# Optimization experiments

Measured on AMD Instinct MI355X. Metric: run time of the kernel, lower is better.

Reference implementation:

```python
import jax, jax.numpy as jnp
import numpy as np

V = 6890   # SMPL vertices
K = 24     # joints
NB = 10    # shape betas
NP = 207   # pose blendshape basis = 23*9
PARENTS = np.array([-1, 0, 0, 0, 1, 2, 3, 4, 5, 6, 7, 8, 9, 9, 9, 12, 13, 14, 16, 17, 18, 19, 20, 21])


def setup_inputs() -> dict:
    key = jax.random.key(0)
    ks = jax.random.split(key, 8)
    B = 1024
    body_pose = jax.random.normal(ks[0], (B, 69), dtype=jnp.float32) * 0.2
    betas = jax.random.normal(ks[1], (B, NB), dtype=jnp.float32)
    global_orient = jax.random.normal(ks[2], (B, 3), dtype=jnp.float32) * 0.2
    v_template = jax.random.normal(ks[3], (V, 3), dtype=jnp.float32) * 0.1
    shapedirs = jax.random.normal(ks[4], (V, 3, NB), dtype=jnp.float32) * 0.01
    posedirs = jax.random.normal(ks[5], (NP, V * 3), dtype=jnp.float32) * 0.01
    J_regressor = jax.nn.softmax(jax.random.normal(ks[6], (K, V), dtype=jnp.float32), axis=-1)
    lbs_weights = jax.nn.softmax(jax.random.normal(ks[7], (V, K), dtype=jnp.float32) * 4.0, axis=-1)
    parents = jnp.asarray(PARENTS, dtype=jnp.int32)
    return dict(body_pose=body_pose, betas=betas, global_orient=global_orient,
                v_template=v_template, shapedirs=shapedirs, posedirs=posedirs,
                J_regressor=J_regressor, lbs_weights=lbs_weights, parents=parents)


def _rodrigues(aa):
    # aa: [..., 3] axis-angle -> [..., 3, 3] rotation matrices
    angle = jnp.linalg.norm(aa + 1e-8, axis=-1, keepdims=True)  # [...,1]
    axis = aa / angle
    sin = jnp.sin(angle)[..., None]
    cos = jnp.cos(angle)[..., None]
    rx, ry, rz = axis[..., 0], axis[..., 1], axis[..., 2]
    z = jnp.zeros_like(rx)
    Km = jnp.stack([z, -rz, ry, rz, z, -rx, -ry, rx, z], axis=-1).reshape(aa.shape[:-1] + (3, 3))
    ident = jnp.eye(3, dtype=aa.dtype)
    return ident + sin * Km + (1.0 - cos) * (Km @ Km)


def reference(body_pose, betas, global_orient, v_template, shapedirs, posedirs,
              J_regressor, lbs_weights, parents):
    full_pose = jnp.concatenate([global_orient, body_pose], axis=1)  # [B,72]
    B = betas.shape[0]
    dtype = betas.dtype

    # shape blend shapes
    v_shaped = v_template + jnp.einsum('bl,vkl->bvk', betas, shapedirs)  # [B,V,3]
    # rest joints
    joints_t = jnp.einsum('jv,bvk->bjk', J_regressor, v_shaped)          # [B,K,3]

    # pose -> rotation matrices (pose2rot=True path)
    rot_mats = _rodrigues(full_pose.reshape(B, K, 3))                    # [B,K,3,3]

    # pose blend shapes
    ident = jnp.eye(3, dtype=dtype)
    pose_feature = (rot_mats[:, 1:] - ident).reshape(B, NP)              # [B,207]
    v_posed = v_shaped + (pose_feature @ posedirs).reshape(B, V, 3)

    # kinematic chain (batch_rigid_transform)
    rel_joints = joints_t.at[:, 1:].add(-joints_t[:, PARENTS[1:]])       # [B,K,3]
    tm = jnp.concatenate([rot_mats, rel_joints[..., None]], axis=-1)     # [B,K,3,4]
    bottom = jnp.broadcast_to(jnp.array([0., 0., 0., 1.], dtype=dtype), (B, K, 1, 4))
    tm = jnp.concatenate([tm, bottom], axis=-2)                          # [B,K,4,4]
    chain = [tm[:, 0]]
    for i in range(1, K):  # fixed small kinematic tree
        chain.append(chain[PARENTS[i]] @ tm[:, i])
    transforms = jnp.stack(chain, axis=1)                                # [B,K,4,4]
    joints = transforms[..., :3, 3]                                      # posed joints

    # relative transforms: subtract rotated rest-joint position
    A = transforms.at[..., :3, 3].add(
        -jnp.einsum('bkij,bkj->bki', transforms[..., :3, :3], joints_t))  # [B,K,4,4]

    # linear blend skinning
    T = jnp.einsum('vk,bkij->bvij', lbs_weights, A)                      # [B,V,4,4]
    vertices = jnp.einsum('bvij,bvj->bvi', T[..., :3, :3], v_posed) + T[..., :3, 3]
    return vertices, joints_t, joints, rot_mats
```

## Files before the change

### kernel.cpp

```cpp
#include <hip/hip_runtime.h>
#include <hip/hip_bf16.h>

#define VNUM 6890
#define KJ 24
#define NBETA 10
#define NPOSE 207
#define KPAD 224
#define BATCH 1024
#define N3 20670
#define NVG 431
#define NROWF 20688

#define OUT_V  0
#define OUT_JT 21166080
#define OUT_J  21239808
#define OUT_RM 21313536

#define WS_JVJS 0
#define WS_ABFF 792
#define WS_WBFF 262936
#define WS_PFBF 373528
#define WS_PDTF 488216

typedef unsigned short ushort;
typedef __attribute__((ext_vector_type(8))) short short8v;
typedef __attribute__((ext_vector_type(4))) float floatx4;

__device__ __forceinline__ ushort f2bfu(float x) {
  __hip_bfloat16 h = __float2bfloat16(x);
  union { __hip_bfloat16 h; ushort u; } cv; cv.h = h; return cv.u;
}

__global__ __launch_bounds__(256) void jreg_kernel(
    const float* __restrict__ Jr, const float* __restrict__ vt,
    const float* __restrict__ sd, float* __restrict__ JvJs) {
  const int j = blockIdx.x;
  const int chunk = blockIdx.y;
  const int t = threadIdx.x;
  const int lane = t & 63, wid = t >> 6;
  const int vbeg = chunk * 1723;
  const int vend = (vbeg + 1723 < VNUM) ? vbeg + 1723 : VNUM;
  __shared__ float red[4][33];
  float acc[33];
#pragma unroll
  for (int q = 0; q < 33; q++) acc[q] = 0.0f;
  for (int v = vbeg + t; v < vend; v += 256) {
    float r = Jr[j * VNUM + v];
    const float* vtp = vt + v * 3;
    const float* sdp = sd + v * 30;
    acc[0] += r * vtp[0];
    acc[1] += r * vtp[1];
    acc[2] += r * vtp[2];
#pragma unroll
    for (int q = 0; q < 30; q++) acc[3 + q] += r * sdp[q];
  }
#pragma unroll
  for (int q = 0; q < 33; q++) {
    float x = acc[q];
    for (int off = 32; off > 0; off >>= 1) x += __shfl_down(x, off, 64);
    if (lane == 0) red[wid][q] = x;
  }
  __syncthreads();
  if (t < 33)
    atomicAdd(&JvJs[j * 33 + t], red[0][t] + red[1][t] + red[2][t] + red[3][t]);
}

__global__ __launch_bounds__(64) void batch_prep(
    const float* __restrict__ body_pose, const float* __restrict__ betas,
    const float* __restrict__ global_orient, const float* __restrict__ JvJs,
    float* __restrict__ out_jt, float* __restrict__ out_j, float* __restrict__ out_rm,
    ushort* __restrict__ pfbf, ushort* __restrict__ Abff) {
  const int b = blockIdx.x;
  const int t = threadIdx.x;
  __shared__ float R[24][9];
  __shared__ float jt[24][3];
  __shared__ float chR[24][9];
  __shared__ float cht[24][3];

  if (t < 24) {
    float ax, ay, az;
    if (t == 0) {
      ax = global_orient[b * 3 + 0];
      ay = global_orient[b * 3 + 1];
      az = global_orient[b * 3 + 2];
    } else {
      const float* p = body_pose + (size_t)b * 69 + (t - 1) * 3;
      ax = p[0]; ay = p[1]; az = p[2];
    }
    float px = ax + 1e-8f, py = ay + 1e-8f, pz = az + 1e-8f;
    float angle = sqrtf(px * px + py * py + pz * pz);
    float inv = 1.0f / angle;
    float rx = ax * inv, ry = ay * inv, rz = az * inv;
    float s = sinf(angle), c = cosf(angle);
    float cc = 1.0f - c;
    float m[9];
    m[0] = 1.0f - cc * (ry * ry + rz * rz);
    m[1] = -s * rz + cc * rx * ry;
    m[2] =  s * ry + cc * rx * rz;
    m[3] =  s * rz + cc * rx * ry;
    m[4] = 1.0f - cc * (rx * rx + rz * rz);
    m[5] = -s * rx + cc * ry * rz;
    m[6] = -s * ry + cc * rx * rz;
    m[7] =  s * rx + cc * ry * rz;
    m[8] = 1.0f - cc * (rx * rx + ry * ry);
#pragma unroll
    for (int e = 0; e < 9; e++) {
      R[t][e] = m[e];
      out_rm[(size_t)b * 216 + t * 9 + e] = m[e];
    }
  }
  for (int idx = t; idx < 72; idx += 64) {
    int j = idx / 3, c = idx % 3;
    const float* JJ = JvJs + j * 33;
    float s = JJ[c];
    const float* be = betas + (size_t)b * NBETA;
#pragma unroll
    for (int l = 0; l < NBETA; l++) s += be[l] * JJ[3 + c * 10 + l];
    jt[j][c] = s;
    out_jt[(size_t)b * 72 + idx] = s;
  }
  __syncthreads();
  for (int mI = t; mI < KPAD; mI += 64) {
    float val = 0.0f;
    if (mI < NPOSE) {
      int k = 1 + mI / 9, e = mI % 9;
      val = R[k][e] - ((e == 0 || e == 4 || e == 8) ? 1.0f : 0.0f);
    } else if (mI < NPOSE + NBETA) {
      val = betas[(size_t)b * NBETA + (mI - NPOSE)];
    }
    int kb = mI >> 5, quad = (mI >> 3) & 3, j = mI & 7;
    pfbf[(size_t)(((b >> 4) * 7 + kb) * 512) + (quad * 16 + (b & 15)) * 8 + j] =
        f2bfu(val);
  }
  if (t == 0) {
    const int par[24] = {-1, 0, 0, 0, 1, 2, 3, 4, 5, 6, 7, 8, 9, 9, 9, 12, 13, 14, 16, 17, 18, 19, 20, 21};
#pragma unroll
    for (int e = 0; e < 9; e++) chR[0][e] = R[0][e];
    cht[0][0] = jt[0][0]; cht[0][1] = jt[0][1]; cht[0][2] = jt[0][2];
    for (int k = 1; k < 24; k++) {
      int p = par[k];
      float rel0 = jt[k][0] - jt[p][0];
      float rel1 = jt[k][1] - jt[p][1];
      float rel2 = jt[k][2] - jt[p][2];
#pragma unroll
      for (int i = 0; i < 3; i++) {
        float a0 = chR[p][i * 3 + 0], a1 = chR[p][i * 3 + 1], a2 = chR[p][i * 3 + 2];
        chR[k][i * 3 + 0] = a0 * R[k][0] + a1 * R[k][3] + a2 * R[k][6];
        chR[k][i * 3 + 1] = a0 * R[k][1] + a1 * R[k][4] + a2 * R[k][7];
        chR[k][i * 3 + 2] = a0 * R[k][2] + a1 * R[k][5] + a2 * R[k][8];
        cht[k][i] = a0 * rel0 + a1 * rel1 + a2 * rel2 + cht[p][i];
      }
    }
  }
  __syncthreads();
  if (t < 24) {
    int k = t;
#pragma unroll
    for (int i = 0; i < 3; i++) out_j[(size_t)b * 72 + k * 3 + i] = cht[k][i];
  }
  for (int e = t; e < 512; e += 64) {
    int quad = e >> 7, n = (e >> 3) & 15, j = e & 7;
    int k = quad * 8 + j;
    float val = 0.0f;
    if (n < 12 && k < 24) {
      int i = n >> 2, jj = n & 3;
      if (jj < 3) {
        val = chR[k][i * 3 + jj];
      } else {
        val = cht[k][i] - (chR[k][i * 3 + 0] * jt[k][0] +
                           chR[k][i * 3 + 1] * jt[k][1] +
                           chR[k][i * 3 + 2] * jt[k][2]);
      }
    }
    Abff[(size_t)b * 512 + e] = f2bfu(val);
  }
}

__global__ __launch_bounds__(256) void transpose_pd(
    const float* __restrict__ pd, ushort* __restrict__ pdTf,
    const float* __restrict__ sd,
    const float* __restrict__ w, ushort* __restrict__ wbff) {
  {
    int lb = blockIdx.y * 324 + blockIdx.x;
    if (lb < 864) {
      int i = lb * 256 + threadIdx.x;
      int vg = i >> 9, e = i & 511;
      int quad = e >> 7, l15 = (e >> 3) & 15, j = e & 7;
      int v = vg * 16 + l15, k = quad * 8 + j;
      float x = (v < VNUM && k < 24) ? w[v * 24 + k] : 0.0f;
      wbff[i] = f2bfu(x);
    }
  }
  __shared__ float tile[32][65];
  const int t = threadIdx.x;
  const int n0 = blockIdx.x * 64;
  const int k0 = blockIdx.y * 32;
  const int c = t & 63;
  for (int r = t >> 6; r < 32; r += 4) {
    int k = k0 + r, n = n0 + c;
    float x = 0.0f;
    if (n < N3) {
      if (k < NPOSE) x = pd[(size_t)k * N3 + n];
      else if (k < NPOSE + NBETA) x = sd[(size_t)n * 10 + (k - NPOSE)];
    }
    tile[r][c] = x;
  }
  __syncthreads();
  const int n = t >> 2;
  const int j0 = (t & 3) * 8;
  const int rg = n0 + n;
  if (rg >= NROWF) return;
  unsigned int outw[4];
#pragma unroll
  for (int jj = 0; jj < 4; jj++) {
    unsigned int lo = f2bfu(tile[j0 + jj * 2][n]);
    unsigned int hi = f2bfu(tile[j0 + jj * 2 + 1][n]);
    outw[jj] = lo | (hi << 16);
  }
  const int vg = rg / 48;
  const int rl = rg - vg * 48;
  const int ns = rl >> 4, l15 = rl & 15;
  const int kb = k0 >> 5, quad = j0 >> 3;
  *(uint4*)&pdTf[(size_t)(((vg * 3 + ns) * 7 + kb) * 512) + (quad * 16 + l15) * 8] =
      make_uint4(outw[0], outw[1], outw[2], outw[3]);
}

__global__ __launch_bounds__(256, 2) void fused_mfma(
    const ushort* __restrict__ pfbf, const ushort* __restrict__ pdTf,
    const float* __restrict__ vt, const ushort* __restrict__ wbff,
    const ushort* __restrict__ Abff, float* __restrict__ out_v) {
  __shared__ __align__(16) ushort AbS[32 * 512];
  __shared__ float vpS[4][32 * 50];
  const int tid = threadIdx.x;
  const int lane = tid & 63, wv = tid >> 6;
  const int l15 = lane & 15, quad = lane >> 4;

  const int bid = blockIdx.x;
  const int L = (bid & 7) * 432 + (bid >> 3);
  const int bt = L & 31;
  const int q  = L >> 5;
  const int bm = bt * 32;
  const int vg = q * 4 + wv;
  const int vgc = (vg < NVG) ? vg : (NVG - 1);

  short8v ab[8];
  {
    const ushort* asrc = Abff + (size_t)(bm + wv * 8) * 512 + lane * 8;
#pragma unroll
    for (int j = 0; j < 8; j++) ab[j] = *(const short8v*)(asrc + j * 512);
  }

  const short8v wf = *(const short8v*)(wbff + (size_t)vgc * 512 + lane * 8);
  const int gn0 = vgc * 48 + l15;
  float vt0 = (gn0      < N3) ? vt[gn0]      : 0.0f;
  float vt1 = (gn0 + 16 < N3) ? vt[gn0 + 16] : 0.0f;
  float vt2 = (gn0 + 32 < N3) ? vt[gn0 + 32] : 0.0f;

  const ushort* apf0 = pfbf + (size_t)((bm >> 4) * 7) * 512 + lane * 8;
  const ushort* apf1 = apf0 + 7 * 512;
  const ushort* bpf  = pdTf + (size_t)(vgc * 21) * 512 + lane * 8;

  const floatx4 zero = {0.0f, 0.0f, 0.0f, 0.0f};
  floatx4 acc[2][3];
#pragma unroll
  for (int bg = 0; bg < 2; bg++)
#pragma unroll
    for (int ns = 0; ns < 3; ns++) acc[bg][ns] = zero;

#pragma unroll
  for (int kb = 0; kb < 7; kb++) {
    short8v a0 = *(const short8v*)(apf0 + kb * 512);
    short8v a1 = *(const short8v*)(apf1 + kb * 512);
    short8v b0 = *(const short8v*)(bpf + (0 * 7 + kb) * 512);
    short8v b1 = *(const short8v*)(bpf + (1 * 7 + kb) * 512);
    short8v b2 = *(const short8v*)(bpf + (2 * 7 + kb) * 512);
    acc[0][0] = __builtin_amdgcn_mfma_f32_16x16x32_bf16(a0, b0, acc[0][0], 0, 0, 0);
    acc[0][1] = __builtin_amdgcn_mfma_f32_16x16x32_bf16(a0, b1, acc[0][1], 0, 0, 0);
    acc[0][2] = __builtin_amdgcn_mfma_f32_16x16x32_bf16(a0, b2, acc[0][2], 0, 0, 0);
    acc[1][0] = __builtin_amdgcn_mfma_f32_16x16x32_bf16(a1, b0, acc[1][0], 0, 0, 0);
    acc[1][1] = __builtin_amdgcn_mfma_f32_16x16x32_bf16(a1, b1, acc[1][1], 0, 0, 0);
    acc[1][2] = __builtin_amdgcn_mfma_f32_16x16x32_bf16(a1, b2, acc[1][2], 0, 0, 0);
  }

  float* myvp = vpS[wv];
#pragma unroll
  for (int bg = 0; bg < 2; bg++) {
#pragma unroll
    for (int r = 0; r < 4; r++) {
      int row = bg * 16 + quad * 4 + r;
      myvp[row * 50 +      l15] = acc[bg][0][r] + vt0;
      myvp[row * 50 + 16 + l15] = acc[bg][1][r] + vt1;
      myvp[row * 50 + 32 + l15] = acc[bg][2][r] + vt2;
    }
  }

  {
    ushort* adst = AbS + (size_t)(wv * 8) * 512 + lane * 8;
#pragma unroll
    for (int j = 0; j < 8; j++) *(short8v*)(adst + j * 512) = ab[j];
  }
  __syncthreads();

  const int gv = vgc * 16 + l15;
  const bool active = (quad < 3) && (vg < NVG) && (gv < VNUM);
  float* outp = out_v + (size_t)bm * N3 + (size_t)gv * 3 + quad;
  const float* pbase = myvp + 3 * l15;

#pragma unroll
  for (int i = 0; i < 32; i++) {
    short8v afrag = *(const short8v*)&AbS[i * 512 + lane * 8];
    floatx4 t = __builtin_amdgcn_mfma_f32_16x16x32_bf16(afrag, wf, zero, 0, 0, 0);
    float px = pbase[i * 50 + 0];
    float py = pbase[i * 50 + 1];
    float pz = pbase[i * 50 + 2];
    if (active) {
      *outp = t[0] * px + t[1] * py + t[2] * pz + t[3];
    }
    outp += N3;
  }
}

extern "C" void kernel_launch(void* const* d_in, const int* in_sizes, int n_in,
                              void* d_out, int out_size, void* d_ws, size_t ws_size,
                              hipStream_t stream) {
  const float* body_pose     = (const float*)d_in[0];
  const float* betas         = (const float*)d_in[1];
  const float* global_orient = (const float*)d_in[2];
  const float* v_template    = (const float*)d_in[3];
  const float* shapedirs     = (const float*)d_in[4];
  const float* posedirs      = (const float*)d_in[5];
  const float* J_regressor   = (const float*)d_in[6];
  const float* lbs_weights   = (const float*)d_in[7];

  float* out = (float*)d_out;
  float* out_v  = out + OUT_V;
  float* out_jt = out + OUT_JT;
  float* out_j  = out + OUT_J;
  float* out_rm = out + OUT_RM;

  float* ws = (float*)d_ws;
  float* JvJs = ws + WS_JVJS;
  ushort* Abff = (ushort*)(ws + WS_ABFF);
  ushort* wbff = (ushort*)(ws + WS_WBFF);
  ushort* pfbf = (ushort*)(ws + WS_PFBF);
  ushort* pdTf = (ushort*)(ws + WS_PDTF);

  hipMemsetAsync(JvJs, 0, KJ * 33 * sizeof(float), stream);
  jreg_kernel<<<dim3(KJ, 4), 256, 0, stream>>>(J_regressor, v_template, shapedirs, JvJs);
  transpose_pd<<<dim3(324, 7), 256, 0, stream>>>(posedirs, pdTf, shapedirs,
                                                 lbs_weights, wbff);
  batch_prep<<<BATCH, 64, 0, stream>>>(body_pose, betas, global_orient, JvJs,
                                       out_jt, out_j, out_rm, pfbf, Abff);
  fused_mfma<<<3456, 256, 0, stream>>>(pfbf, pdTf, v_template, wbff, Abff, out_v);
}
```

Baseline: 197.1 us.

## Repartition skinning epilogue by batch row per wave, drop A LDS staging

The skinning phase is reorganised so each wave handles 8 batch rows across all 4 vertex groups of the block, instead of its own vertex group across all 32 batch rows. Each wave now feeds its own preloaded A fragments straight into the MFMA, which removes the AbS shared-memory staging buffer. In exchange it holds four weight fragments and reads other waves' posed vertices through shared memory. The posed-vertex tile is re-laid out padded to vec4 per vertex so it can be read with one float4 load, and launch bounds are raised to 4 blocks per CU to use the freed LDS and registers. The price is more scattered global stores per instruction and tighter register budgets.

```diff
diff --git a/kernel.cpp b/kernel.cpp
--- a/kernel.cpp
+++ b/kernel.cpp
@@ -225,12 +225,11 @@
       make_uint4(outw[0], outw[1], outw[2], outw[3]);
 }
 
-__global__ __launch_bounds__(256, 2) void fused_mfma(
+__global__ __launch_bounds__(256, 4) void fused_mfma(
     const ushort* __restrict__ pfbf, const ushort* __restrict__ pdTf,
     const float* __restrict__ vt, const ushort* __restrict__ wbff,
     const ushort* __restrict__ Abff, float* __restrict__ out_v) {
-  __shared__ __align__(16) ushort AbS[32 * 512];
-  __shared__ float vpS[4][32 * 50];
+  __shared__ float vpS[4 * 32 * 68];
   const int tid = threadIdx.x;
   const int lane = tid & 63, wv = tid >> 6;
   const int l15 = lane & 15, quad = lane >> 4;
@@ -243,14 +242,12 @@
   const int vg = q * 4 + wv;
   const int vgc = (vg < NVG) ? vg : (NVG - 1);
 
-  short8v ab[8];
-  {
-    const ushort* asrc = Abff + (size_t)(bm + wv * 8) * 512 + lane * 8;
-#pragma unroll
-    for (int j = 0; j < 8; j++) ab[j] = *(const short8v*)(asrc + j * 512);
-  }
-
-  const short8v wf = *(const short8v*)(wbff + (size_t)vgc * 512 + lane * 8);
+  short8v wf[4];
+#pragma unroll
+  for (int v4 = 0; v4 < 4; v4++) {
+    int g = q * 4 + v4; if (g >= NVG) g = NVG - 1;
+    wf[v4] = *(const short8v*)(wbff + (size_t)g * 512 + lane * 8);
+  }
   const int gn0 = vgc * 48 + l15;
   float vt0 = (gn0      < N3) ? vt[gn0]      : 0.0f;
   float vt1 = (gn0 + 16 < N3) ? vt[gn0 + 16] : 0.0f;
@@ -282,41 +279,57 @@
     acc[1][2] = __builtin_amdgcn_mfma_f32_16x16x32_bf16(a1, b2, acc[1][2], 0, 0, 0);
   }
 
-  float* myvp = vpS[wv];
+  float* myvp = vpS + wv * 2176;
+  int v_[3], c_[3];
+#pragma unroll
+  for (int ns = 0; ns < 3; ns++) {
+    int col = ns * 16 + l15;
+    v_[ns] = col / 3;
+    c_[ns] = col - v_[ns] * 3;
+  }
 #pragma unroll
   for (int bg = 0; bg < 2; bg++) {
 #pragma unroll
     for (int r = 0; r < 4; r++) {
       int row = bg * 16 + quad * 4 + r;
-      myvp[row * 50 +      l15] = acc[bg][0][r] + vt0;
-      myvp[row * 50 + 16 + l15] = acc[bg][1][r] + vt1;
-      myvp[row * 50 + 32 + l15] = acc[bg][2][r] + vt2;
-    }
-  }
-
+      myvp[row * 68 + v_[0] * 4 + c_[0]] = acc[bg][0][r] + vt0;
+      myvp[row * 68 + v_[1] * 4 + c_[1]] = acc[bg][1][r] + vt1;
+      myvp[row * 68 + v_[2] * 4 + c_[2]] = acc[bg][2][r] + vt2;
+    }
+  }
+
+  short8v apre[8];
   {
-    ushort* adst = AbS + (size_t)(wv * 8) * 512 + lane * 8;
-#pragma unroll
-    for (int j = 0; j < 8; j++) *(short8v*)(adst + j * 512) = ab[j];
-  }
-  __syncthreads();
-
-  const int gv = vgc * 16 + l15;
-  const bool active = (quad < 3) && (vg < NVG) && (gv < VNUM);
-  float* outp = out_v + (size_t)bm * N3 + (size_t)gv * 3 + quad;
-  const float* pbase = myvp + 3 * l15;
-
-#pragma unroll
-  for (int i = 0; i < 32; i++) {
-    short8v afrag = *(const short8v*)&AbS[i * 512 + lane * 8];
-    floatx4 t = __builtin_amdgcn_mfma_f32_16x16x32_bf16(afrag, wf, zero, 0, 0, 0);
-    float px = pbase[i * 50 + 0];
-    float py = pbase[i * 50 + 1];
-    float pz = pbase[i * 50 + 2];
-    if (active) {
-      *outp = t[0] * px + t[1] * py + t[2] * pz + t[3];
-    }
-    outp += N3;
+    const ushort* abase = Abff + (size_t)(bm + wv * 8) * 512 + lane * 8;
+#pragma unroll
+    for (int j = 0; j < 8; j++) apre[j] = *(const short8v*)(abase + j * 512);
+  }
+
+  __syncthreads();
+
+  bool act[4];
+  int gvv[4];
+#pragma unroll
+  for (int v4 = 0; v4 < 4; v4++) {
+    int vg2 = q * 4 + v4;
+    gvv[v4] = vg2 * 16 + l15;
+    act[v4] = (quad < 3) && (vg2 < NVG) && (gvv[v4] < VNUM);
+  }
+
+#pragma unroll
+  for (int i = 0; i < 8; i++) {
+    const int b = wv * 8 + i;
+    const size_t gb = (size_t)(bm + b);
+    short8v afrag = apre[i];
+#pragma unroll
+    for (int v4 = 0; v4 < 4; v4++) {
+      floatx4 t = __builtin_amdgcn_mfma_f32_16x16x32_bf16(afrag, wf[v4], zero, 0, 0, 0);
+      const float4 p = *(const float4*)&vpS[v4 * 2176 + b * 68 + l15 * 4];
+      if (act[v4]) {
+        out_v[gb * N3 + (size_t)gvv[v4] * 3 + quad] =
+            t[0] * p.x + t[1] * p.y + t[2] * p.z + t[3];
+      }
+    }
   }
 }
 
```

Result: faster. 182.3 us (-7.5%).
